# Performance work log

Measured on AMD Instinct MI355X. Metric: run time of the kernel, lower is better.

The kernel has to match this reference:

```python
import jax, jax.numpy as jnp
import numpy as np

N = 100000   # num_nodes
E = 1600000  # num_edges (avg degree 16)
D = 64       # embed_channels
C = 16       # num_classes
EPSILON = 0.1  # AntiSymmetricConv step size (PyG default)
GAMMA = 0.1    # AntiSymmetricConv diffusion strength (PyG default)


def setup_inputs() -> dict:
    key = jax.random.key(0)
    ks = jax.random.split(key, 9)
    s = 1.0 / np.sqrt(D)
    return {
        "edge_index": jax.random.randint(ks[0], (2, E), 0, N, dtype=jnp.int32),
        "embed_w": jax.random.normal(ks[1], (N, D), dtype=jnp.float32) * 0.1,
        "W_rel": jax.random.normal(ks[2], (D, D), dtype=jnp.float32) * s,   # GraphConv lin_rel weight
        "b_rel": jax.random.normal(ks[3], (D,), dtype=jnp.float32) * s,     # GraphConv lin_rel bias
        "W_root": jax.random.normal(ks[4], (D, D), dtype=jnp.float32) * s,  # GraphConv lin_root weight (no bias)
        "W_anti": jax.random.normal(ks[5], (D, D), dtype=jnp.float32) * s,  # AntiSymmetricConv W
        "b_anti": jax.random.normal(ks[6], (D,), dtype=jnp.float32) * s,    # AntiSymmetricConv bias
        "W_lin": jax.random.normal(ks[7], (C, D), dtype=jnp.float32) * s,   # lin2 weight
        "b_lin": jax.random.normal(ks[8], (C,), dtype=jnp.float32) * s,     # lin2 bias
    }


def reference(edge_index, embed_w, W_rel, b_rel, W_root, W_anti, b_anti, W_lin, b_lin):
    x = embed_w  # [N, D] node features = embedding table
    src, dst = edge_index[0], edge_index[1]
    # phi = GraphConv with 'add' aggregation: lin_rel(sum_j x_j) + lin_root(x)
    agg = jax.ops.segment_sum(x[src], dst, num_segments=N)  # [N, D] sparse gather+scatter-add
    h = agg @ W_rel.T + b_rel + x @ W_root.T
    # antisymmetric weight: W - W^T - gamma * I
    aW = W_anti - W_anti.T - GAMMA * jnp.eye(D, dtype=x.dtype)
    h = x @ aW.T + h + b_anti
    h = jnp.tanh(h)                       # default act of AntiSymmetricConv
    x = x + EPSILON * h                   # single iteration (num_iters=1 default)
    # dropout p=0.0 -> identity
    out = jax.nn.sigmoid(x @ W_lin.T + b_lin)  # [N, C]
    return out
```

## Files before the change

kernel.cpp:

```cpp
#include <hip/hip_runtime.h>
#include <hip/hip_fp16.h>

#define DD 64
#define CC 16
#define EPSILON 0.1f
#define GAMMA 0.1f
#define BSH 6
#define BSZ 64
#define CAP 1280
#define MAXBK 2048
#define PADH 33
#define PADW 65
#define CSH 10
#define MAXNC 128
#define CAPC 20480
#define L1CHUNK 2048
#define L1THR 512
#define NSLICE 8
#define SRTSZ 2560

__global__ __launch_bounds__(L1THR) void bin_coarse_conv(
        const int* __restrict__ ei, int* __restrict__ gcntc,
        unsigned* __restrict__ binned_c, int E,
        const float* __restrict__ x, __half2* __restrict__ xh2, int N) {
    __shared__ unsigned sorted[SRTSZ];
    __shared__ unsigned char bkt[SRTSZ];
    __shared__ int hist[MAXNC], ph[MAXNC], base[MAXNC], cur[MAXNC], gbase[MAXNC];
    __shared__ int mtot;
    const int t = threadIdx.x;
    if (t < MAXNC) hist[t] = 0;
    __syncthreads();
    const int e0 = blockIdx.x * L1CHUNK;
    unsigned ent[L1CHUNK / L1THR];
    int cbk[L1CHUNK / L1THR];
#pragma unroll
    for (int i = 0; i < L1CHUNK / L1THR; ++i) {
        int e = e0 + t + L1THR * i;
        cbk[i] = -1;
        if (e < E) {
            int src = ei[e], dst = ei[E + e];
            cbk[i] = dst >> CSH;
            ent[i] = (unsigned)src | ((unsigned)(dst & ((1 << CSH) - 1)) << 17);
            atomicAdd(&hist[cbk[i]], 1);
        }
    }
    __syncthreads();
    if (t < MAXNC) { ph[t] = (hist[t] + 3) & ~3; cur[t] = ph[t]; }
    __syncthreads();
    for (int off = 1; off < MAXNC; off <<= 1) {
        int v = 0;
        if (t < MAXNC && t >= off) v = cur[t - off];
        __syncthreads();
        if (t < MAXNC) cur[t] += v;
        __syncthreads();
    }
    if (t < MAXNC) {
        base[t] = cur[t] - ph[t];
        if (t == MAXNC - 1) mtot = cur[t];
        cur[t] = base[t];
    }
    __syncthreads();
#pragma unroll
    for (int i = 0; i < L1CHUNK / L1THR; ++i)
        if (cbk[i] >= 0) {
            int pos = atomicAdd(&cur[cbk[i]], 1);
            sorted[pos] = ent[i];
            bkt[pos] = (unsigned char)cbk[i];
        }
    __syncthreads();
    if (t < MAXNC) {
        int b0 = base[t] + hist[t], b1 = base[t] + ph[t];
        for (int p = b0; p < b1; ++p) {
            sorted[p] = 0xFFFFFFFFu;
            bkt[p] = (unsigned char)t;
        }
        gbase[t] = ph[t] ? atomicAdd(&gcntc[t], ph[t]) : 0;
    }
    __syncthreads();
    const int m = mtot;
    for (int j4 = 4 * t; j4 < m; j4 += 4 * L1THR) {
        int cb = bkt[j4];
        int gp = gbase[cb] + (j4 - base[cb]);
        if (gp + 4 <= CAPC) {
            uint4 v = *(const uint4*)&sorted[j4];
            *(uint4*)&binned_c[(size_t)cb * CAPC + gp] = v;
        }
    }
    const float2* x2 = (const float2*)x;
    const int M = N * (DD / 2);
    const int G = gridDim.x * L1THR;
    for (int i = blockIdx.x * L1THR + t; i < M; i += G)
        xh2[i] = __float22half2_rn(x2[i]);
}

__global__ __launch_bounds__(256) void bin_fine_w(
        const int* __restrict__ gcntc, const unsigned* __restrict__ binned_c,
        int* __restrict__ gcnt, unsigned* __restrict__ binned,
        const float* __restrict__ Wrel, const float* __restrict__ Wroot,
        const float* __restrict__ Wanti, const float* __restrict__ brel,
        const float* __restrict__ banti,
        float* __restrict__ B_g, float* __restrict__ bc) {
    const int t = threadIdx.x;
    if (blockIdx.x == gridDim.x - 1) {
        for (int idx = t; idx < 128 * 64; idx += 256) {
            int k = idx >> 6, d = idx & 63;
            float v;
            if (k < 64) {
                v = Wrel[d * 64 + k];
            } else {
                int j = k - 64;
                v = Wroot[d * 64 + j] + Wanti[d * 64 + j] - Wanti[j * 64 + d];
                if (d == j) v -= GAMMA;
            }
            B_g[idx] = v;
        }
        if (t < 64) bc[t] = brel[t] + banti[t];
        return;
    }
    __shared__ int hist[16];
    __shared__ int hbase[16];
    const int c = blockIdx.x >> 3, s = blockIdx.x & (NSLICE - 1);
    int cnt = gcntc[c];
    if (cnt > CAPC) cnt = CAPC;
    const int per = (cnt + NSLICE - 1) / NSLICE;
    const int i0 = s * per;
    int i1 = i0 + per;
    if (i1 > cnt) i1 = cnt;
    if (t < 16) hist[t] = 0;
    __syncthreads();
    const unsigned* bcp = binned_c + (size_t)c * CAPC;
    unsigned ent[10];
#pragma unroll
    for (int j = 0; j < 10; ++j) {
        int i = i0 + t + j * 256;
        ent[j] = (i < i1) ? bcp[i] : 0xFFFFFFFFu;
        if (ent[j] != 0xFFFFFFFFu) atomicAdd(&hist[ent[j] >> (17 + BSH)], 1);
    }
    __syncthreads();
    if (t < 16) {
        hbase[t] = hist[t] ? atomicAdd(&gcnt[c * 16 + t], hist[t]) : 0;
        hist[t] = 0;
    }
    __syncthreads();
#pragma unroll
    for (int j = 0; j < 10; ++j) {
        if (ent[j] != 0xFFFFFFFFu) {
            unsigned dstc = ent[j] >> 17;
            int f = dstc >> BSH;
            int pos = hbase[f] + atomicAdd(&hist[f], 1);
            if (pos < CAP)
                binned[(size_t)(c * 16 + f) * CAP + pos] =
                    (ent[j] & 0x1FFFF) | ((dstc & (BSZ - 1)) << 17);
        }
    }
}

__global__ __launch_bounds__(512, 8) void mega(
        const __half* __restrict__ x_h,
        const int* __restrict__ gcnt, const unsigned* __restrict__ binned,
        const float* __restrict__ B_g, const float* __restrict__ bc,
        const float* __restrict__ Wlin, const float* __restrict__ blin,
        float* __restrict__ out, int N) {
    __shared__ __half2 R0h[BSZ * PADH];
    __shared__ float wl_sh[CC * PADW];
    __shared__ int csr[CAP];
    __shared__ int deg[BSZ], offs[BSZ], cur[BSZ];

    const int t = threadIdx.x;
    const int b = blockIdx.x;
    const int nb0 = b << BSH;
    int cnt = gcnt[b];
    if (cnt > CAP) cnt = CAP;
    const unsigned* bl = binned + (size_t)b * CAP;

#pragma unroll
    for (int i = 0; i < 2; ++i) {
        int idx = t + 512 * i;
        wl_sh[(idx >> 6) * PADW + (idx & 63)] = Wlin[idx];
    }
    if (t < BSZ) deg[t] = 0;
    __syncthreads();
    for (int i = t; i < cnt; i += 512) atomicAdd(&deg[bl[i] >> 17], 1);
    __syncthreads();
    if (t < BSZ) offs[t] = deg[t];
    __syncthreads();
    for (int off = 1; off < BSZ; off <<= 1) {
        int v = 0;
        if (t < BSZ && t >= off) v = offs[t - off];
        __syncthreads();
        if (t < BSZ) offs[t] += v;
        __syncthreads();
    }
    if (t < BSZ) {
        int ex = offs[t] - deg[t];
        offs[t] = ex;
        cur[t] = ex;
    }
    __syncthreads();
    for (int i = t; i < cnt; i += 512) {
        unsigned en = bl[i];
        int pos = atomicAdd(&cur[en >> 17], 1);
        csr[pos] = (int)(en & 0x1FFFF);
    }
    __syncthreads();

    {
        const int g = t >> 3, q = t & 7;
        const float4* xh4 = (const float4*)x_h;
        const int i0 = offs[g], dc = deg[g];
        __half2 z = __floats2half2_rn(0.f, 0.f);
        __half2 A0[4] = {z, z, z, z}, A1[4] = {z, z, z, z};
        int i = 0;
        for (; i + 2 <= dc; i += 2) {
            int s0 = csr[i0 + i], s1 = csr[i0 + i + 1];
            float4 v0 = xh4[s0 * 8 + q];
            float4 v1 = xh4[s1 * 8 + q];
            const __half2* h0 = (const __half2*)&v0;
            const __half2* h1 = (const __half2*)&v1;
#pragma unroll
            for (int rr = 0; rr < 4; ++rr) {
                A0[rr] = __hadd2(A0[rr], h0[rr]);
                A1[rr] = __hadd2(A1[rr], h1[rr]);
            }
        }
        if (i < dc) {
            int s0 = csr[i0 + i];
            float4 v0 = xh4[s0 * 8 + q];
            const __half2* h0 = (const __half2*)&v0;
#pragma unroll
            for (int rr = 0; rr < 4; ++rr) A0[rr] = __hadd2(A0[rr], h0[rr]);
        }
        __half2* row = &R0h[g * PADH + 4 * q];
#pragma unroll
        for (int rr = 0; rr < 4; ++rr) row[rr] = __hadd2(A0[rr], A1[rr]);
    }
    __syncthreads();

    const int nl = t & 63;
    const int dg = __builtin_amdgcn_readfirstlane(t >> 6);
    float acc[8];
#pragma unroll
    for (int j = 0; j < 8; ++j) acc[j] = 0.f;
#pragma unroll 8
    for (int kk = 0; kk < 32; ++kk) {
        float2 af = __half22float2(R0h[nl * PADH + kk]);
        const float* B0 = &B_g[(2 * kk) * DD + dg * 8];
        const float* B1 = &B_g[(2 * kk + 1) * DD + dg * 8];
#pragma unroll
        for (int j = 0; j < 8; ++j) acc[j] = fmaf(af.x, B0[j], acc[j]);
#pragma unroll
        for (int j = 0; j < 8; ++j) acc[j] = fmaf(af.y, B1[j], acc[j]);
    }
    __syncthreads();

    {
        int nn = N - nb0;
        if (nn > BSZ) nn = BSZ;
        const float4* xh4 = (const float4*)x_h;
        for (int idx = t; idx < nn * 8; idx += 512) {
            float4 v = xh4[(size_t)nb0 * 8 + idx];
            const __half2* h = (const __half2*)&v;
            __half2* row = &R0h[(idx >> 3) * PADH + (idx & 7) * 4];
            row[0] = h[0]; row[1] = h[1]; row[2] = h[2]; row[3] = h[3];
        }
    }
    __syncthreads();

#pragma unroll 8
    for (int kk = 0; kk < 32; ++kk) {
        float2 af = __half22float2(R0h[nl * PADH + kk]);
        const float* B0 = &B_g[(64 + 2 * kk) * DD + dg * 8];
        const float* B1 = &B_g[(64 + 2 * kk + 1) * DD + dg * 8];
#pragma unroll
        for (int j = 0; j < 8; ++j) acc[j] = fmaf(af.x, B0[j], acc[j]);
#pragma unroll
        for (int j = 0; j < 8; ++j) acc[j] = fmaf(af.y, B1[j], acc[j]);
    }

#pragma unroll
    for (int jj = 0; jj < 4; ++jj) {
        int d2 = dg * 4 + jj;
        float2 xf = __half22float2(R0h[nl * PADH + d2]);
        float h0 = acc[2 * jj] + bc[2 * d2];
        float h1 = acc[2 * jj + 1] + bc[2 * d2 + 1];
        float th0 = 1.0f - 2.0f / (__expf(2.0f * h0) + 1.0f);
        float th1 = 1.0f - 2.0f / (__expf(2.0f * h1) + 1.0f);
        acc[2 * jj] = xf.x + EPSILON * th0;
        acc[2 * jj + 1] = xf.y + EPSILON * th1;
    }
    __syncthreads();
#pragma unroll
    for (int jj = 0; jj < 4; ++jj)
        R0h[nl * PADH + dg * 4 + jj] =
            __floats2half2_rn(acc[2 * jj], acc[2 * jj + 1]);
    __syncthreads();

    {
        const int g = t >> 3, q = t & 7;
        const int n = nb0 + g;
        if (n < N) {
            float p0 = blin[2 * q], p1 = blin[2 * q + 1];
#pragma unroll 8
            for (int d2 = 0; d2 < 32; ++d2) {
                float2 xf = __half22float2(R0h[g * PADH + d2]);
                p0 = fmaf(xf.x, wl_sh[(2 * q) * PADW + 2 * d2], p0);
                p0 = fmaf(xf.y, wl_sh[(2 * q) * PADW + 2 * d2 + 1], p0);
                p1 = fmaf(xf.x, wl_sh[(2 * q + 1) * PADW + 2 * d2], p1);
                p1 = fmaf(xf.y, wl_sh[(2 * q + 1) * PADW + 2 * d2 + 1], p1);
            }
            float2 o;
            o.x = 1.0f / (1.0f + __expf(-p0));
            o.y = 1.0f / (1.0f + __expf(-p1));
            *(float2*)(out + (size_t)n * CC + 2 * q) = o;
        }
    }
}

extern "C" void kernel_launch(void* const* d_in, const int* in_sizes, int n_in,
                              void* d_out, int out_size, void* d_ws, size_t ws_size,
                              hipStream_t stream) {
    const int*   ei    = (const int*)d_in[0];
    const float* x     = (const float*)d_in[1];
    const float* Wrel  = (const float*)d_in[2];
    const float* brel  = (const float*)d_in[3];
    const float* Wroot = (const float*)d_in[4];
    const float* Wanti = (const float*)d_in[5];
    const float* banti = (const float*)d_in[6];
    const float* Wlin  = (const float*)d_in[7];
    const float* blin  = (const float*)d_in[8];
    float* out = (float*)d_out;

    const int E = in_sizes[0] / 2;
    const int N = in_sizes[1] / DD;
    const int NC = (N + (1 << CSH) - 1) >> CSH;

    __half* x_h = (__half*)d_ws;
    unsigned* binned_c = (unsigned*)(x_h + (size_t)N * DD);
    unsigned* binned = binned_c + (size_t)MAXNC * CAPC;
    int*   gcntc = (int*)(binned + (size_t)MAXBK * CAP);
    int*   gcnt  = gcntc + MAXNC;
    float* B_g   = (float*)(gcnt + MAXBK);
    float* bc    = B_g + 128 * 64;

    hipMemsetAsync(gcntc, 0, (MAXNC + MAXBK) * sizeof(int), stream);
    bin_coarse_conv<<<(E + L1CHUNK - 1) / L1CHUNK, L1THR, 0, stream>>>(
        ei, gcntc, binned_c, E, x, (__half2*)x_h, N);
    bin_fine_w<<<NC * NSLICE + 1, 256, 0, stream>>>(
        gcntc, binned_c, gcnt, binned, Wrel, Wroot, Wanti, brel, banti, B_g, bc);
    mega<<<NC * 16, 512, 0, stream>>>(x_h, gcnt, binned, B_g, bc, Wlin, blin, out, N);
}
```

Before: 182.6 us.

## Gather neighbor features in FP8 and keep shared tile in fp32

Node features are quantized to FP8 (e4m3 via packed convert) instead of fp16, which halves the bytes fetched per neighbor in the random gather, the dominant memory cost. Gathered values are accumulated in fp32, the shared-memory tile switches from half2 to fp32, and the root/self term reads the original fp32 features directly. The fp32 tile doubles LDS use per block, which can lower occupancy, and FP8 quantization of x adds numerical error to the aggregated sum.

```diff
diff --git a/kernel.cpp b/kernel.cpp
--- a/kernel.cpp
+++ b/kernel.cpp
@@ -1,5 +1,4 @@
 #include <hip/hip_runtime.h>
-#include <hip/hip_fp16.h>
 
 #define DD 64
 #define CC 16
@@ -9,7 +8,7 @@
 #define BSZ 64
 #define CAP 1280
 #define MAXBK 2048
-#define PADH 33
+#define PAD 65
 #define PADW 65
 #define CSH 10
 #define MAXNC 128
@@ -19,10 +18,12 @@
 #define NSLICE 8
 #define SRTSZ 2560
 
+typedef float v2f __attribute__((ext_vector_type(2)));
+
 __global__ __launch_bounds__(L1THR) void bin_coarse_conv(
         const int* __restrict__ ei, int* __restrict__ gcntc,
         unsigned* __restrict__ binned_c, int E,
-        const float* __restrict__ x, __half2* __restrict__ xh2, int N) {
+        const float* __restrict__ x, unsigned* __restrict__ x_q, int N) {
     __shared__ unsigned sorted[SRTSZ];
     __shared__ unsigned char bkt[SRTSZ];
     __shared__ int hist[MAXNC], ph[MAXNC], base[MAXNC], cur[MAXNC], gbase[MAXNC];
@@ -86,11 +87,15 @@
             *(uint4*)&binned_c[(size_t)cb * CAPC + gp] = v;
         }
     }
-    const float2* x2 = (const float2*)x;
-    const int M = N * (DD / 2);
+    const float4* x4 = (const float4*)x;
+    const int M = N * (DD / 4);
     const int G = gridDim.x * L1THR;
-    for (int i = blockIdx.x * L1THR + t; i < M; i += G)
-        xh2[i] = __float22half2_rn(x2[i]);
+    for (int i = blockIdx.x * L1THR + t; i < M; i += G) {
+        float4 a = x4[i];
+        int r = __builtin_amdgcn_cvt_pk_fp8_f32(a.x, a.y, 0, false);
+        r = __builtin_amdgcn_cvt_pk_fp8_f32(a.z, a.w, r, true);
+        x_q[i] = (unsigned)r;
+    }
 }
 
 __global__ __launch_bounds__(256) void bin_fine_w(
@@ -156,12 +161,12 @@
 }
 
 __global__ __launch_bounds__(512, 8) void mega(
-        const __half* __restrict__ x_h,
+        const float* __restrict__ x, const unsigned* __restrict__ x_q,
         const int* __restrict__ gcnt, const unsigned* __restrict__ binned,
         const float* __restrict__ B_g, const float* __restrict__ bc,
         const float* __restrict__ Wlin, const float* __restrict__ blin,
         float* __restrict__ out, int N) {
-    __shared__ __half2 R0h[BSZ * PADH];
+    __shared__ float R0[BSZ * PAD];
     __shared__ float wl_sh[CC * PADW];
     __shared__ int csr[CAP];
     __shared__ int deg[BSZ], offs[BSZ], cur[BSZ];
@@ -206,33 +211,38 @@
 
     {
         const int g = t >> 3, q = t & 7;
-        const float4* xh4 = (const float4*)x_h;
+        const uint2* xq2 = (const uint2*)x_q;
         const int i0 = offs[g], dc = deg[g];
-        __half2 z = __floats2half2_rn(0.f, 0.f);
-        __half2 A0[4] = {z, z, z, z}, A1[4] = {z, z, z, z};
+        float a0[8], a1[8];
+#pragma unroll
+        for (int r = 0; r < 8; ++r) { a0[r] = 0.f; a1[r] = 0.f; }
         int i = 0;
         for (; i + 2 <= dc; i += 2) {
             int s0 = csr[i0 + i], s1 = csr[i0 + i + 1];
-            float4 v0 = xh4[s0 * 8 + q];
-            float4 v1 = xh4[s1 * 8 + q];
-            const __half2* h0 = (const __half2*)&v0;
-            const __half2* h1 = (const __half2*)&v1;
-#pragma unroll
-            for (int rr = 0; rr < 4; ++rr) {
-                A0[rr] = __hadd2(A0[rr], h0[rr]);
-                A1[rr] = __hadd2(A1[rr], h1[rr]);
-            }
+            uint2 v0 = xq2[s0 * 8 + q];
+            uint2 v1 = xq2[s1 * 8 + q];
+            v2f f;
+            f = __builtin_amdgcn_cvt_pk_f32_fp8(v0.x, false); a0[0] += f.x; a0[1] += f.y;
+            f = __builtin_amdgcn_cvt_pk_f32_fp8(v0.x, true);  a0[2] += f.x; a0[3] += f.y;
+            f = __builtin_amdgcn_cvt_pk_f32_fp8(v0.y, false); a0[4] += f.x; a0[5] += f.y;
+            f = __builtin_amdgcn_cvt_pk_f32_fp8(v0.y, true);  a0[6] += f.x; a0[7] += f.y;
+            f = __builtin_amdgcn_cvt_pk_f32_fp8(v1.x, false); a1[0] += f.x; a1[1] += f.y;
+            f = __builtin_amdgcn_cvt_pk_f32_fp8(v1.x, true);  a1[2] += f.x; a1[3] += f.y;
+            f = __builtin_amdgcn_cvt_pk_f32_fp8(v1.y, false); a1[4] += f.x; a1[5] += f.y;
+            f = __builtin_amdgcn_cvt_pk_f32_fp8(v1.y, true);  a1[6] += f.x; a1[7] += f.y;
         }
         if (i < dc) {
             int s0 = csr[i0 + i];
-            float4 v0 = xh4[s0 * 8 + q];
-            const __half2* h0 = (const __half2*)&v0;
-#pragma unroll
-            for (int rr = 0; rr < 4; ++rr) A0[rr] = __hadd2(A0[rr], h0[rr]);
-        }
-        __half2* row = &R0h[g * PADH + 4 * q];
-#pragma unroll
-        for (int rr = 0; rr < 4; ++rr) row[rr] = __hadd2(A0[rr], A1[rr]);
+            uint2 v0 = xq2[s0 * 8 + q];
+            v2f f;
+            f = __builtin_amdgcn_cvt_pk_f32_fp8(v0.x, false); a0[0] += f.x; a0[1] += f.y;
+            f = __builtin_amdgcn_cvt_pk_f32_fp8(v0.x, true);  a0[2] += f.x; a0[3] += f.y;
+            f = __builtin_amdgcn_cvt_pk_f32_fp8(v0.y, false); a0[4] += f.x; a0[5] += f.y;
+            f = __builtin_amdgcn_cvt_pk_f32_fp8(v0.y, true);  a0[6] += f.x; a0[7] += f.y;
+        }
+        float* row = &R0[g * PAD + 8 * q];
+#pragma unroll
+        for (int r = 0; r < 8; ++r) row[r] = a0[r] + a1[r];
     }
     __syncthreads();
 
@@ -242,57 +252,45 @@
 #pragma unroll
     for (int j = 0; j < 8; ++j) acc[j] = 0.f;
 #pragma unroll 8
-    for (int kk = 0; kk < 32; ++kk) {
-        float2 af = __half22float2(R0h[nl * PADH + kk]);
-        const float* B0 = &B_g[(2 * kk) * DD + dg * 8];
-        const float* B1 = &B_g[(2 * kk + 1) * DD + dg * 8];
-#pragma unroll
-        for (int j = 0; j < 8; ++j) acc[j] = fmaf(af.x, B0[j], acc[j]);
-#pragma unroll
-        for (int j = 0; j < 8; ++j) acc[j] = fmaf(af.y, B1[j], acc[j]);
+    for (int k = 0; k < DD; ++k) {
+        float a = R0[nl * PAD + k];
+        const float* Bk = &B_g[k * DD + dg * 8];
+#pragma unroll
+        for (int j = 0; j < 8; ++j) acc[j] = fmaf(a, Bk[j], acc[j]);
     }
     __syncthreads();
 
     {
         int nn = N - nb0;
         if (nn > BSZ) nn = BSZ;
-        const float4* xh4 = (const float4*)x_h;
-        for (int idx = t; idx < nn * 8; idx += 512) {
-            float4 v = xh4[(size_t)nb0 * 8 + idx];
-            const __half2* h = (const __half2*)&v;
-            __half2* row = &R0h[(idx >> 3) * PADH + (idx & 7) * 4];
-            row[0] = h[0]; row[1] = h[1]; row[2] = h[2]; row[3] = h[3];
+        const float4* x4 = (const float4*)x;
+        for (int idx = t; idx < nn * 16; idx += 512) {
+            float4 v = x4[nb0 * 16 + idx];
+            float* row = &R0[(idx >> 4) * PAD + (idx & 15) * 4];
+            row[0] = v.x; row[1] = v.y; row[2] = v.z; row[3] = v.w;
         }
     }
     __syncthreads();
 
 #pragma unroll 8
-    for (int kk = 0; kk < 32; ++kk) {
-        float2 af = __half22float2(R0h[nl * PADH + kk]);
-        const float* B0 = &B_g[(64 + 2 * kk) * DD + dg * 8];
-        const float* B1 = &B_g[(64 + 2 * kk + 1) * DD + dg * 8];
-#pragma unroll
-        for (int j = 0; j < 8; ++j) acc[j] = fmaf(af.x, B0[j], acc[j]);
-#pragma unroll
-        for (int j = 0; j < 8; ++j) acc[j] = fmaf(af.y, B1[j], acc[j]);
-    }
-
-#pragma unroll
-    for (int jj = 0; jj < 4; ++jj) {
-        int d2 = dg * 4 + jj;
-        float2 xf = __half22float2(R0h[nl * PADH + d2]);
-        float h0 = acc[2 * jj] + bc[2 * d2];
-        float h1 = acc[2 * jj + 1] + bc[2 * d2 + 1];
-        float th0 = 1.0f - 2.0f / (__expf(2.0f * h0) + 1.0f);
-        float th1 = 1.0f - 2.0f / (__expf(2.0f * h1) + 1.0f);
-        acc[2 * jj] = xf.x + EPSILON * th0;
-        acc[2 * jj + 1] = xf.y + EPSILON * th1;
-    }
-    __syncthreads();
-#pragma unroll
-    for (int jj = 0; jj < 4; ++jj)
-        R0h[nl * PADH + dg * 4 + jj] =
-            __floats2half2_rn(acc[2 * jj], acc[2 * jj + 1]);
+    for (int k = 0; k < DD; ++k) {
+        float a = R0[nl * PAD + k];
+        const float* Bk = &B_g[(DD + k) * DD + dg * 8];
+#pragma unroll
+        for (int j = 0; j < 8; ++j) acc[j] = fmaf(a, Bk[j], acc[j]);
+    }
+
+#pragma unroll
+    for (int j = 0; j < 8; ++j) {
+        int d = dg * 8 + j;
+        float h = acc[j] + bc[d];
+        float e2 = __expf(2.0f * h);
+        float th = 1.0f - 2.0f / (e2 + 1.0f);
+        acc[j] = R0[nl * PAD + d] + EPSILON * th;
+    }
+    __syncthreads();
+#pragma unroll
+    for (int j = 0; j < 8; ++j) R0[nl * PAD + dg * 8 + j] = acc[j];
     __syncthreads();
 
     {
@@ -301,12 +299,10 @@
         if (n < N) {
             float p0 = blin[2 * q], p1 = blin[2 * q + 1];
 #pragma unroll 8
-            for (int d2 = 0; d2 < 32; ++d2) {
-                float2 xf = __half22float2(R0h[g * PADH + d2]);
-                p0 = fmaf(xf.x, wl_sh[(2 * q) * PADW + 2 * d2], p0);
-                p0 = fmaf(xf.y, wl_sh[(2 * q) * PADW + 2 * d2 + 1], p0);
-                p1 = fmaf(xf.x, wl_sh[(2 * q + 1) * PADW + 2 * d2], p1);
-                p1 = fmaf(xf.y, wl_sh[(2 * q + 1) * PADW + 2 * d2 + 1], p1);
+            for (int d = 0; d < DD; ++d) {
+                float xv = R0[g * PAD + d];
+                p0 = fmaf(xv, wl_sh[(2 * q) * PADW + d], p0);
+                p1 = fmaf(xv, wl_sh[(2 * q + 1) * PADW + d], p1);
             }
             float2 o;
             o.x = 1.0f / (1.0f + __expf(-p0));
@@ -334,8 +330,8 @@
     const int N = in_sizes[1] / DD;
     const int NC = (N + (1 << CSH) - 1) >> CSH;
 
-    __half* x_h = (__half*)d_ws;
-    unsigned* binned_c = (unsigned*)(x_h + (size_t)N * DD);
+    unsigned* x_q = (unsigned*)d_ws;
+    unsigned* binned_c = x_q + (size_t)N * (DD / 4);
     unsigned* binned = binned_c + (size_t)MAXNC * CAPC;
     int*   gcntc = (int*)(binned + (size_t)MAXBK * CAP);
     int*   gcnt  = gcntc + MAXNC;
@@ -344,8 +340,8 @@
 
     hipMemsetAsync(gcntc, 0, (MAXNC + MAXBK) * sizeof(int), stream);
     bin_coarse_conv<<<(E + L1CHUNK - 1) / L1CHUNK, L1THR, 0, stream>>>(
-        ei, gcntc, binned_c, E, x, (__half2*)x_h, N);
+        ei, gcntc, binned_c, E, x, x_q, N);
     bin_fine_w<<<NC * NSLICE + 1, 256, 0, stream>>>(
         gcntc, binned_c, gcnt, binned, Wrel, Wroot, Wanti, brel, banti, B_g, bc);
-    mega<<<NC * 16, 512, 0, stream>>>(x_h, gcnt, binned, B_g, bc, Wlin, blin, out, N);
+    mega<<<NC * 16, 512, 0, stream>>>(x, x_q, gcnt, binned, B_g, bc, Wlin, blin, out, N);
 }
```

Result: faster. 174.8 us (-4.3%).
